# Optimization experiments

Measured on AMD Instinct MI355X. Metric: run time of the kernel, lower is better.

Reference implementation:

```python
import jax, jax.numpy as jnp
import numpy as np

N_HEAD = 16
D_MODEL = 1024
B, C = 4, 2048

def setup_inputs() -> dict:
    key = jax.random.key(0)
    k_x, k_wq, k_bq, k_wo, k_bo = jax.random.split(key, 5)
    s = 0.02
    return {
        "x": jax.random.normal(k_x, (B, C, D_MODEL), dtype=jnp.float32),
        "W_qkv": jax.random.normal(k_wq, (D_MODEL, 3 * D_MODEL), dtype=jnp.float32) * s,
        "b_qkv": jax.random.normal(k_bq, (3 * D_MODEL,), dtype=jnp.float32) * s,
        "W_o": jax.random.normal(k_wo, (D_MODEL, D_MODEL), dtype=jnp.float32) * s,
        "b_o": jax.random.normal(k_bo, (D_MODEL,), dtype=jnp.float32) * s,
    }

def reference(x, W_qkv, b_qkv, W_o, b_o):
    Bsz, Cq, D = x.shape
    H = N_HEAD
    hd = D // H
    qkv = x @ W_qkv + b_qkv                      # [B,C,3D]
    Q, K, V = jnp.split(qkv, 3, axis=2)
    # [B,C,H,hd] -> [B,H,C,hd]
    Q = Q.reshape(Bsz, Cq, H, hd).transpose(0, 2, 1, 3)
    K = K.reshape(Bsz, Cq, H, hd).transpose(0, 2, 1, 3)
    V = V.reshape(Bsz, Cq, H, hd).transpose(0, 2, 1, 3)
    scale = 1.0 / np.sqrt(hd).astype(np.float32)
    att = jnp.einsum('bhqd,bhkd->bhqk', Q, K) * scale
    causal = jnp.tril(jnp.ones((Cq, Cq), dtype=bool))
    att = jnp.where(causal, att, jnp.float32(-jnp.inf))
    att = jax.nn.softmax(att, axis=-1)           # dropout = identity (eval)
    out = jnp.einsum('bhqk,bhkd->bhqd', att, V)  # [B,H,C,hd]
    out = out.transpose(0, 2, 1, 3).reshape(Bsz, Cq, D)
    return out @ W_o + b_o
```

## Files before the change

### kernel.cpp

```cpp
#include <hip/hip_runtime.h>
#include <hip/hip_bf16.h>

typedef __attribute__((ext_vector_type(8))) short bf16x8;
typedef __attribute__((ext_vector_type(4))) float f32x4;

#define NH 16
#define DM 1024
#define HD 64
#define CSEQ 2048
#define MROWS 8192
#define NBH 64

static __device__ __forceinline__ unsigned short f2bf(float f) {
  __hip_bfloat16 h = __float2bfloat16(f);
  return *reinterpret_cast<unsigned short*>(&h);
}

static __device__ __forceinline__ short bf_qscale(short s) {
  unsigned u = ((unsigned)(unsigned short)s) << 16;
  float f = __builtin_bit_cast(float, u) * 0.18033688f;
  return (short)f2bf(f);
}

static __device__ __forceinline__ void gload_lds16(const void* g, void* l) {
  __builtin_amdgcn_global_load_lds(
      (const __attribute__((address_space(1))) unsigned int*)g,
      (__attribute__((address_space(3))) unsigned int*)l, 16, 0, 0);
}

__global__ __launch_bounds__(256) void cast_f32_bf16(const float* __restrict__ in,
                                                     unsigned short* __restrict__ out,
                                                     int n4) {
  int stride = gridDim.x * blockDim.x;
  for (int i = blockIdx.x * blockDim.x + threadIdx.x; i < n4; i += stride) {
    float4 v = ((const float4*)in)[i];
    ushort4 o;
    o.x = f2bf(v.x); o.y = f2bf(v.y); o.z = f2bf(v.z); o.w = f2bf(v.w);
    ((ushort4*)out)[i] = o;
  }
}

__global__ __launch_bounds__(256) void transpose_cast(const float* __restrict__ src,
                                                      unsigned short* __restrict__ dst,
                                                      int K, int N) {
  __shared__ float tile[32][33];
  int tx = threadIdx.x, ty = threadIdx.y;
  int n0 = blockIdx.x * 32, k0 = blockIdx.y * 32;
  #pragma unroll
  for (int i = 0; i < 32; i += 8)
    tile[ty + i][tx] = src[(size_t)(k0 + ty + i) * N + n0 + tx];
  __syncthreads();
  #pragma unroll
  for (int i = 0; i < 32; i += 8)
    dst[(size_t)(n0 + ty + i) * K + k0 + tx] = f2bf(tile[tx][ty + i]);
}


static __device__ __forceinline__ void stage_half(const unsigned short* s0,
                                                  const unsigned short* s1,
                                                  char* dst, int c0, int c1) {
  gload_lds16(s0, dst + c0 * 16);
  gload_lds16(s1, dst + c1 * 16);
}

template<int CNT>
static __device__ __forceinline__ void ld_frags(const char* base, int r0, int cx, int g,
                                                bf16x8 (*out)[2]) {
  #pragma unroll
  for (int i = 0; i < CNT; i++) {
    int row = r0 + i * 16 + cx;
    #pragma unroll
    for (int kc = 0; kc < 2; kc++)
      out[i][kc] = *(const bf16x8*)(base + row * 128 + ((((kc << 2) | g) ^ (row & 7)) << 4));
  }
}

static __device__ __forceinline__ void mfma_q(const bf16x8 af[4][2], const bf16x8 bfr[2][2],
                                              f32x4 acc[8][4], int qm, int qn) {
  #pragma unroll
  for (int kc = 0; kc < 2; kc++)
    #pragma unroll
    for (int mi = 0; mi < 4; mi++)
      #pragma unroll
      for (int ni = 0; ni < 2; ni++)
        acc[qm * 4 + mi][qn * 2 + ni] = __builtin_amdgcn_mfma_f32_16x16x32_bf16(
            af[mi][kc], bfr[ni][kc], acc[qm * 4 + mi][qn * 2 + ni], 0, 0, 0);
}

#define BARR() __builtin_amdgcn_s_barrier()
#define LGKM0() asm volatile("s_waitcnt lgkmcnt(0)" ::: "memory")
#define PRIO1() __builtin_amdgcn_s_setprio(1)
#define PRIO0() __builtin_amdgcn_s_setprio(0)

template<int MODE>
__global__ __launch_bounds__(512, 2) void gemm256(const unsigned short* __restrict__ A,
                                                  const unsigned short* __restrict__ BT,
                                                  const float* __restrict__ bias,
                                                  float* __restrict__ outF,
                                                  unsigned short* __restrict__ outQKV,
                                                  int N, int K) {
  __shared__ char sA[2][32768];
  __shared__ char sB[2][32768];
  int tid = threadIdx.x;
  int w = tid >> 6, l = tid & 63, g = l >> 4, cx = l & 15;
  int wm = (w >> 2) * 128, wn = (w & 3) * 64;

  int nwgx = gridDim.x;
  int nwg = nwgx * gridDim.y;
  int gid = blockIdx.y * nwgx + blockIdx.x;
  int swz = (gid & 7) * (nwg >> 3) + (gid >> 3);
  int bm = (swz / nwgx) * 256, bn = (swz % nwgx) * 256;

  int c0 = tid, c1 = tid + 512;
  int ar0 = c0 >> 3, as0 = ((c0 & 7) ^ (ar0 & 7)) * 8;
  int ar1 = c1 >> 3, as1 = ((c1 & 7) ^ (ar1 & 7)) * 8;
  const unsigned short* Ap0 = A + (size_t)(bm + ar0) * K + as0;
  const unsigned short* Ap1 = A + (size_t)(bm + ar1) * K + as1;
  const unsigned short* Bp0 = BT + (size_t)(bn + ar0) * K + as0;
  const unsigned short* Bp1 = BT + (size_t)(bn + ar1) * K + as1;
  const size_t HS = (size_t)128 * K;

  f32x4 acc[8][4];
  #pragma unroll
  for (int i = 0; i < 8; i++)
    #pragma unroll
    for (int j = 0; j < 4; j++) acc[i][j] = (f32x4){0.f, 0.f, 0.f, 0.f};

  int NT = K >> 6;

  stage_half(Ap0,      Ap1,      sA[0],         c0, c1);
  stage_half(Ap0 + HS, Ap1 + HS, sA[0] + 16384, c0, c1);
  stage_half(Bp0,      Bp1,      sB[0],         c0, c1);
  stage_half(Bp0 + HS, Bp1 + HS, sB[0] + 16384, c0, c1);
  stage_half(Ap0 + 64, Ap1 + 64, sA[1],         c0, c1);
  asm volatile("s_waitcnt vmcnt(2)" ::: "memory");
  BARR();

  int cur = 0;
  for (int t = 0; t < NT; t++) {
    const char* Ac = sA[cur];
    const char* Bc = sB[cur];
    char* An = sA[cur ^ 1];
    char* Bn = sB[cur ^ 1];
    int kn  = (t + 1) << 6;
    int kn2 = (t + 2) << 6;
    bool h1 = (t + 1) < NT, h2 = (t + 2) < NT;
    bf16x8 af[4][2], bfr[2][2];

    ld_frags<4>(Ac, wm, cx, g, af);
    ld_frags<2>(Bc, wn, cx, g, bfr);
    if (h1) stage_half(Ap0 + HS + kn, Ap1 + HS + kn, An + 16384, c0, c1);
    BARR(); LGKM0();
    PRIO1(); mfma_q(af, bfr, acc, 0, 0); PRIO0();
    BARR();

    ld_frags<2>(Bc, wn + 32, cx, g, bfr);
    if (h1) stage_half(Bp0 + kn, Bp1 + kn, Bn, c0, c1);
    BARR(); LGKM0();
    PRIO1(); mfma_q(af, bfr, acc, 0, 1); PRIO0();
    BARR();

    ld_frags<4>(Ac, wm + 64, cx, g, af);
    ld_frags<2>(Bc, wn, cx, g, bfr);
    if (h1) stage_half(Bp0 + HS + kn, Bp1 + HS + kn, Bn + 16384, c0, c1);
    BARR(); LGKM0();
    PRIO1(); mfma_q(af, bfr, acc, 1, 0); PRIO0();
    BARR();

    ld_frags<2>(Bc, wn + 32, cx, g, bfr);
    BARR(); LGKM0();
    if (h2) stage_half(Ap0 + kn2, Ap1 + kn2, sA[cur], c0, c1);
    PRIO1(); mfma_q(af, bfr, acc, 1, 1); PRIO0();
    if (h1) {
      if (h2) { asm volatile("s_waitcnt vmcnt(2)" ::: "memory"); }
      else    { asm volatile("s_waitcnt vmcnt(0)" ::: "memory"); }
    }
    BARR();
    cur ^= 1;
  }

  #pragma unroll
  for (int ai = 0; ai < 8; ai++) {
    #pragma unroll
    for (int aj = 0; aj < 4; aj++) {
      int col = bn + wn + aj * 16 + cx;
      float bv = bias[col];
      int row0 = bm + wm + ai * 16 + g * 4;
      #pragma unroll
      for (int r = 0; r < 4; r++) {
        float v = acc[ai][aj][r] + bv;
        int rr = row0 + r;
        if (MODE == 0) {
          outF[(size_t)rr * N + col] = v;
        } else {
          int which = col >> 10, rem = col & 1023;
          int h = rem >> 6, d = rem & 63;
          int b = rr >> 11, cq = rr & 2047;
          if (which == 2) {
            int pos = (cq & ~31) + (((cq >> 2) & 3) << 3) + (((cq >> 4) & 1) << 2) + (cq & 3);
            outQKV[((size_t)2 * NBH + b * NH + h) * (CSEQ * HD) +
                   (size_t)d * CSEQ + pos] = f2bf(v);
          } else {
            outQKV[((size_t)which * NBH + b * NH + h) * (CSEQ * HD) + (size_t)cq * HD + d] = f2bf(v);
          }
        }
      }
    }
  }
}

__global__ __launch_bounds__(512, 4) void attn_kernel(const unsigned short* __restrict__ Qb,
                                                      const unsigned short* __restrict__ Kb,
                                                      const unsigned short* __restrict__ VTb,
                                                      unsigned short* __restrict__ O) {
  __shared__ char sKb[2][16384];
  __shared__ char sVt[2][16384];
  int tid = threadIdx.x;
  int w = tid >> 6, l = tid & 63, g = l >> 4, cx = l & 15;
  int gid = blockIdx.x;
  int bh = ((gid >> 7) << 3) | (gid & 7);
  int qt = 15 - ((gid >> 3) & 15);

  const unsigned short* Qp  = Qb  + (size_t)bh * CSEQ * HD;
  const unsigned short* Kp  = Kb  + (size_t)bh * CSEQ * HD;
  const unsigned short* VTp = VTb + (size_t)bh * CSEQ * HD;

  int qrow = qt * 128 + w * 16 + cx;
  bf16x8 qf[2];
  qf[0] = *(const bf16x8*)(Qp + (size_t)qrow * HD + g * 8);
  qf[1] = *(const bf16x8*)(Qp + (size_t)qrow * HD + 32 + g * 8);
  #pragma unroll
  for (int kc = 0; kc < 2; kc++)
    #pragma unroll
    for (int j = 0; j < 8; j++) qf[kc][j] = bf_qscale(qf[kc][j]);

  f32x4 o[4];
  #pragma unroll
  for (int nf2 = 0; nf2 < 4; nf2++) o[nf2] = (f32x4){0.f, 0.f, 0.f, 0.f};
  float mrow = -INFINITY, lrow = 0.f;

  int c0 = tid, c1 = tid + 512;
  int krow0 = c0 >> 3, ksl0 = (c0 & 7) ^ (krow0 & 7);
  int krow1 = c1 >> 3, ksl1 = (c1 & 7) ^ (krow1 & 7);
  int vd0 = c0 >> 4, vsl0 = (c0 & 15) ^ (vd0 & 7);
  int vd1 = c1 >> 4, vsl1 = (c1 & 15) ^ (vd1 & 7);
  const unsigned short* Ksrc0 = Kp + (size_t)krow0 * HD + ksl0 * 8;
  const unsigned short* Ksrc1 = Kp + (size_t)krow1 * HD + ksl1 * 8;
  const unsigned short* Vsrc0 = VTp + (size_t)vd0 * CSEQ + vsl0 * 8;
  const unsigned short* Vsrc1 = VTp + (size_t)vd1 * CSEQ + vsl1 * 8;

  gload_lds16(Ksrc0, sKb[0] + c0 * 16);
  gload_lds16(Ksrc1, sKb[0] + c1 * 16);
  gload_lds16(Vsrc0, sVt[0] + c0 * 16);
  gload_lds16(Vsrc1, sVt[0] + c1 * 16);
  __syncthreads();
  int cur = 0;

  for (int kt = 0; kt <= qt; kt++) {
    if (kt < qt) {
      size_t ko = (size_t)(kt + 1) * 128 * HD;
      size_t vo = (size_t)(kt + 1) * 128;
      gload_lds16(Ksrc0 + ko, sKb[cur ^ 1] + c0 * 16);
      gload_lds16(Ksrc1 + ko, sKb[cur ^ 1] + c1 * 16);
      gload_lds16(Vsrc0 + vo, sVt[cur ^ 1] + c0 * 16);
      gload_lds16(Vsrc1 + vo, sVt[cur ^ 1] + c1 * 16);
    }
    const char* Kc = sKb[cur];
    const char* Vc = sVt[cur];

    f32x4 sacc[8];
    #pragma unroll
    for (int nf = 0; nf < 8; nf++) sacc[nf] = (f32x4){0.f, 0.f, 0.f, 0.f};
    __builtin_amdgcn_s_setprio(1);
    #pragma unroll
    for (int kc = 0; kc < 2; kc++) {
      #pragma unroll
      for (int nf = 0; nf < 8; nf++) {
        int row = nf * 16 + cx;
        bf16x8 kf = *(const bf16x8*)(Kc + row * 128 + ((((kc << 2) | g) ^ (row & 7)) << 4));
        sacc[nf] = __builtin_amdgcn_mfma_f32_16x16x32_bf16(kf, qf[kc], sacc[nf], 0, 0, 0);
      }
    }
    __builtin_amdgcn_s_setprio(0);

    if (kt == qt) {
      #pragma unroll
      for (int nf = 0; nf < 8; nf++)
        #pragma unroll
        for (int r = 0; r < 4; r++)
          if (nf * 16 + 4 * g + r > w * 16 + cx) sacc[nf][r] = -INFINITY;
    }
    float m8[8];
    #pragma unroll
    for (int nf = 0; nf < 8; nf++)
      m8[nf] = fmaxf(fmaxf(sacc[nf][0], sacc[nf][1]), fmaxf(sacc[nf][2], sacc[nf][3]));
    float mx = fmaxf(fmaxf(fmaxf(m8[0], m8[1]), fmaxf(m8[2], m8[3])),
                     fmaxf(fmaxf(m8[4], m8[5]), fmaxf(m8[6], m8[7])));
    mx = fmaxf(mx, __shfl_xor(mx, 16));
    mx = fmaxf(mx, __shfl_xor(mx, 32));

    if (!__all(mx - mrow <= 8.f)) {
      float mnew = fmaxf(mrow, mx);
      float alpha = __builtin_amdgcn_exp2f(mrow - mnew);
      mrow = mnew;
      lrow *= alpha;
      #pragma unroll
      for (int r = 0; r < 4; r++) {
        float ar = __shfl(alpha, (l & 48) | ((l >> 2) & 12) | r);
        #pragma unroll
        for (int nf2 = 0; nf2 < 4; nf2++) o[nf2][r] *= ar;
      }
    }
    #pragma unroll
    for (int nf = 0; nf < 8; nf++)
      #pragma unroll
      for (int r = 0; r < 4; r++)
        sacc[nf][r] = __builtin_amdgcn_exp2f(sacc[nf][r] - mrow);
    float s8[8];
    #pragma unroll
    for (int nf = 0; nf < 8; nf++)
      s8[nf] = (sacc[nf][0] + sacc[nf][1]) + (sacc[nf][2] + sacc[nf][3]);
    float sum = ((s8[0] + s8[1]) + (s8[2] + s8[3])) + ((s8[4] + s8[5]) + (s8[6] + s8[7]));
    sum += __shfl_xor(sum, 16);
    sum += __shfl_xor(sum, 32);
    lrow += sum;

    bf16x8 pa[4];
    #pragma unroll
    for (int kc = 0; kc < 4; kc++) {
      #pragma unroll
      for (int j = 0; j < 4; j++) {
        pa[kc][j]     = (short)f2bf(sacc[2 * kc][j]);
        pa[kc][j + 4] = (short)f2bf(sacc[2 * kc + 1][j]);
      }
    }

    __builtin_amdgcn_s_setprio(1);
    #pragma unroll
    for (int kc = 0; kc < 4; kc++) {
      #pragma unroll
      for (int nf2 = 0; nf2 < 4; nf2++) {
        int d = nf2 * 16 + cx;
        bf16x8 vf = *(const bf16x8*)(Vc + ((d * 256 + (((kc << 2) | g) << 4)) ^ ((d & 7) << 4)));
        o[nf2] = __builtin_amdgcn_mfma_f32_16x16x32_bf16(pa[kc], vf, o[nf2], 0, 0, 0);
      }
    }
    __builtin_amdgcn_s_setprio(0);

    if (kt < qt) {
      __syncthreads();
      cur ^= 1;
    }
  }

  int b = bh >> 4, h = bh & 15;
  float linv = 1.0f / lrow;
  #pragma unroll
  for (int r = 0; r < 4; r++) {
    float inv = __shfl(linv, (l & 48) | ((l >> 2) & 12) | r);
    int q = qt * 128 + w * 16 + 4 * g + r;
    size_t base = ((size_t)(b * CSEQ + q)) * DM + h * HD;
    #pragma unroll
    for (int nf2 = 0; nf2 < 4; nf2++)
      O[base + nf2 * 16 + cx] = f2bf(o[nf2][r] * inv);
  }
}

extern "C" void kernel_launch(void* const* d_in, const int* in_sizes, int n_in,
                              void* d_out, int out_size, void* d_ws, size_t ws_size,
                              hipStream_t stream) {
  const float* x    = (const float*)d_in[0];
  const float* Wqkv = (const float*)d_in[1];
  const float* bqkv = (const float*)d_in[2];
  const float* Wo   = (const float*)d_in[3];
  const float* bo   = (const float*)d_in[4];
  float* out = (float*)d_out;

  unsigned short* ws = (unsigned short*)d_ws;
  const size_t XB_OFF    = 0;
  const size_t WQKVT_OFF = 8388608;
  const size_t WOT_OFF   = WQKVT_OFF + 3145728;
  const size_t QKV_OFF   = WOT_OFF + 1048576;
  const size_t ATT_OFF   = QKV_OFF + 3 * 8388608;

  unsigned short* xb    = ws + XB_OFF;
  unsigned short* wqkvT = ws + WQKVT_OFF;
  unsigned short* woT   = ws + WOT_OFF;
  unsigned short* qkv   = ws + QKV_OFF;
  unsigned short* att   = ws + ATT_OFF;

  cast_f32_bf16<<<2048, 256, 0, stream>>>(x, xb, (MROWS * DM) / 4);
  transpose_cast<<<dim3(3 * DM / 32, DM / 32), dim3(32, 8), 0, stream>>>(Wqkv, wqkvT, DM, 3 * DM);
  transpose_cast<<<dim3(DM / 32, DM / 32), dim3(32, 8), 0, stream>>>(Wo, woT, DM, DM);

  gemm256<1><<<dim3(3 * DM / 256, MROWS / 256), 512, 0, stream>>>(
      xb, wqkvT, bqkv, nullptr, qkv, 3 * DM, DM);

  attn_kernel<<<dim3(1024), 512, 0, stream>>>(
      qkv, qkv + 8388608, qkv + 16777216, att);

  gemm256<0><<<dim3(DM / 256, MROWS / 256), 512, 0, stream>>>(
      att, woT, bo, out, nullptr, DM, DM);
}
```

Measured before the change: 225.0 us.

## Shrink GEMM tile to 256x128 with 4x2 wave layout and two-phase pipeline

The GEMM block tile changes from 256x256 to 256x128. The 8 waves are rearranged into a 4x2 grid, each owning a 64x64 sub-tile, so per-wave accumulators drop from 128 to 64 floats and B shared memory is halved. The k-loop is reorganized into two MFMA phases with new staging and vmcnt accounting, and the launch grids are doubled. This doubles the block count (notably for the output projection, 128 to 256 blocks), improving occupancy and wave balance across CUs, at the cost of lower arithmetic intensity per block and more A-tile reloads.

```diff
diff --git a/kernel.cpp b/kernel.cpp
--- a/kernel.cpp
+++ b/kernel.cpp
@@ -56,13 +56,6 @@
 }
 
 
-static __device__ __forceinline__ void stage_half(const unsigned short* s0,
-                                                  const unsigned short* s1,
-                                                  char* dst, int c0, int c1) {
-  gload_lds16(s0, dst + c0 * 16);
-  gload_lds16(s1, dst + c1 * 16);
-}
-
 template<int CNT>
 static __device__ __forceinline__ void ld_frags(const char* base, int r0, int cx, int g,
                                                 bf16x8 (*out)[2]) {
@@ -75,20 +68,22 @@
   }
 }
 
-static __device__ __forceinline__ void mfma_q(const bf16x8 af[4][2], const bf16x8 bfr[2][2],
-                                              f32x4 acc[8][4], int qm, int qn) {
+static __device__ __forceinline__ void mfma_pair(const bf16x8 af[4][2], const bf16x8 bf2[2][2],
+                                                 f32x4 acc[4][4], int n0) {
   #pragma unroll
   for (int kc = 0; kc < 2; kc++)
     #pragma unroll
     for (int mi = 0; mi < 4; mi++)
       #pragma unroll
       for (int ni = 0; ni < 2; ni++)
-        acc[qm * 4 + mi][qn * 2 + ni] = __builtin_amdgcn_mfma_f32_16x16x32_bf16(
-            af[mi][kc], bfr[ni][kc], acc[qm * 4 + mi][qn * 2 + ni], 0, 0, 0);
+        acc[mi][n0 + ni] = __builtin_amdgcn_mfma_f32_16x16x32_bf16(
+            af[mi][kc], bf2[ni][kc], acc[mi][n0 + ni], 0, 0, 0);
 }
 
 #define BARR() __builtin_amdgcn_s_barrier()
 #define LGKM0() asm volatile("s_waitcnt lgkmcnt(0)" ::: "memory")
+#define VMCNT4() asm volatile("s_waitcnt vmcnt(4)" ::: "memory")
+#define VMCNT0() asm volatile("s_waitcnt vmcnt(0)" ::: "memory")
 #define PRIO1() __builtin_amdgcn_s_setprio(1)
 #define PRIO0() __builtin_amdgcn_s_setprio(0)
 
@@ -100,16 +95,16 @@
                                                   unsigned short* __restrict__ outQKV,
                                                   int N, int K) {
   __shared__ char sA[2][32768];
-  __shared__ char sB[2][32768];
+  __shared__ char sB[2][16384];
   int tid = threadIdx.x;
   int w = tid >> 6, l = tid & 63, g = l >> 4, cx = l & 15;
-  int wm = (w >> 2) * 128, wn = (w & 3) * 64;
+  int wm = (w >> 1) * 64, wn = (w & 1) * 64;
 
   int nwgx = gridDim.x;
   int nwg = nwgx * gridDim.y;
   int gid = blockIdx.y * nwgx + blockIdx.x;
   int swz = (gid & 7) * (nwg >> 3) + (gid >> 3);
-  int bm = (swz / nwgx) * 256, bn = (swz % nwgx) * 256;
+  int bm = (swz / nwgx) * 256, bn = (swz % nwgx) * 128;
 
   int c0 = tid, c1 = tid + 512;
   int ar0 = c0 >> 3, as0 = ((c0 & 7) ^ (ar0 & 7)) * 8;
@@ -120,75 +115,63 @@
   const unsigned short* Bp1 = BT + (size_t)(bn + ar1) * K + as1;
   const size_t HS = (size_t)128 * K;
 
-  f32x4 acc[8][4];
-  #pragma unroll
-  for (int i = 0; i < 8; i++)
+  #define STAGE_A(t, buf) do { int ko = (t) << 6;                       \
+      gload_lds16(Ap0 + ko,      sA[buf] + c0 * 16);                    \
+      gload_lds16(Ap1 + ko,      sA[buf] + c1 * 16);                    \
+      gload_lds16(Ap0 + HS + ko, sA[buf] + 16384 + c0 * 16);            \
+      gload_lds16(Ap1 + HS + ko, sA[buf] + 16384 + c1 * 16); } while (0)
+  #define STAGE_B(t, buf) do { int ko = (t) << 6;                       \
+      gload_lds16(Bp0 + ko, sB[buf] + c0 * 16);                         \
+      gload_lds16(Bp1 + ko, sB[buf] + c1 * 16); } while (0)
+
+  f32x4 acc[4][4];
+  #pragma unroll
+  for (int i = 0; i < 4; i++)
     #pragma unroll
     for (int j = 0; j < 4; j++) acc[i][j] = (f32x4){0.f, 0.f, 0.f, 0.f};
 
   int NT = K >> 6;
 
-  stage_half(Ap0,      Ap1,      sA[0],         c0, c1);
-  stage_half(Ap0 + HS, Ap1 + HS, sA[0] + 16384, c0, c1);
-  stage_half(Bp0,      Bp1,      sB[0],         c0, c1);
-  stage_half(Bp0 + HS, Bp1 + HS, sB[0] + 16384, c0, c1);
-  stage_half(Ap0 + 64, Ap1 + 64, sA[1],         c0, c1);
-  asm volatile("s_waitcnt vmcnt(2)" ::: "memory");
+  STAGE_A(0, 0);
+  STAGE_B(0, 0);
+  STAGE_A(1, 1);
+  VMCNT4();
   BARR();
 
   int cur = 0;
   for (int t = 0; t < NT; t++) {
     const char* Ac = sA[cur];
     const char* Bc = sB[cur];
-    char* An = sA[cur ^ 1];
-    char* Bn = sB[cur ^ 1];
-    int kn  = (t + 1) << 6;
-    int kn2 = (t + 2) << 6;
     bool h1 = (t + 1) < NT, h2 = (t + 2) < NT;
-    bf16x8 af[4][2], bfr[2][2];
+    bf16x8 af[4][2], bfr[4][2];
 
     ld_frags<4>(Ac, wm, cx, g, af);
-    ld_frags<2>(Bc, wn, cx, g, bfr);
-    if (h1) stage_half(Ap0 + HS + kn, Ap1 + HS + kn, An + 16384, c0, c1);
+    ld_frags<2>(Bc, wn, cx, g, &bfr[0]);
+    if (h1) STAGE_B(t + 1, cur ^ 1);
     BARR(); LGKM0();
-    PRIO1(); mfma_q(af, bfr, acc, 0, 0); PRIO0();
+    PRIO1(); mfma_pair(af, &bfr[0], acc, 0); PRIO0();
     BARR();
 
-    ld_frags<2>(Bc, wn + 32, cx, g, bfr);
-    if (h1) stage_half(Bp0 + kn, Bp1 + kn, Bn, c0, c1);
+    ld_frags<2>(Bc, wn + 32, cx, g, &bfr[2]);
+    if (h2) STAGE_A(t + 2, cur);
     BARR(); LGKM0();
-    PRIO1(); mfma_q(af, bfr, acc, 0, 1); PRIO0();
-    BARR();
-
-    ld_frags<4>(Ac, wm + 64, cx, g, af);
-    ld_frags<2>(Bc, wn, cx, g, bfr);
-    if (h1) stage_half(Bp0 + HS + kn, Bp1 + HS + kn, Bn + 16384, c0, c1);
-    BARR(); LGKM0();
-    PRIO1(); mfma_q(af, bfr, acc, 1, 0); PRIO0();
-    BARR();
-
-    ld_frags<2>(Bc, wn + 32, cx, g, bfr);
-    BARR(); LGKM0();
-    if (h2) stage_half(Ap0 + kn2, Ap1 + kn2, sA[cur], c0, c1);
-    PRIO1(); mfma_q(af, bfr, acc, 1, 1); PRIO0();
-    if (h1) {
-      if (h2) { asm volatile("s_waitcnt vmcnt(2)" ::: "memory"); }
-      else    { asm volatile("s_waitcnt vmcnt(0)" ::: "memory"); }
-    }
+    PRIO1(); mfma_pair(af, &bfr[2], acc, 2); PRIO0();
+    if (h2)      { VMCNT4(); }
+    else if (h1) { VMCNT0(); }
     BARR();
     cur ^= 1;
   }
 
   #pragma unroll
-  for (int ai = 0; ai < 8; ai++) {
-    #pragma unroll
-    for (int aj = 0; aj < 4; aj++) {
-      int col = bn + wn + aj * 16 + cx;
+  for (int mi = 0; mi < 4; mi++) {
+    #pragma unroll
+    for (int ni = 0; ni < 4; ni++) {
+      int col = bn + wn + ni * 16 + cx;
       float bv = bias[col];
-      int row0 = bm + wm + ai * 16 + g * 4;
+      int row0 = bm + wm + mi * 16 + g * 4;
       #pragma unroll
       for (int r = 0; r < 4; r++) {
-        float v = acc[ai][aj][r] + bv;
+        float v = acc[mi][ni][r] + bv;
         int rr = row0 + r;
         if (MODE == 0) {
           outF[(size_t)rr * N + col] = v;
@@ -207,6 +190,8 @@
       }
     }
   }
+  #undef STAGE_A
+  #undef STAGE_B
 }
 
 __global__ __launch_bounds__(512, 4) void attn_kernel(const unsigned short* __restrict__ Qb,
@@ -393,12 +378,12 @@
   transpose_cast<<<dim3(3 * DM / 32, DM / 32), dim3(32, 8), 0, stream>>>(Wqkv, wqkvT, DM, 3 * DM);
   transpose_cast<<<dim3(DM / 32, DM / 32), dim3(32, 8), 0, stream>>>(Wo, woT, DM, DM);
 
-  gemm256<1><<<dim3(3 * DM / 256, MROWS / 256), 512, 0, stream>>>(
+  gemm256<1><<<dim3(3 * DM / 128, MROWS / 256), 512, 0, stream>>>(
       xb, wqkvT, bqkv, nullptr, qkv, 3 * DM, DM);
 
   attn_kernel<<<dim3(1024), 512, 0, stream>>>(
       qkv, qkv + 8388608, qkv + 16777216, att);
 
-  gemm256<0><<<dim3(DM / 256, MROWS / 256), 512, 0, stream>>>(
+  gemm256<0><<<dim3(DM / 128, MROWS / 256), 512, 0, stream>>>(
       att, woT, bo, out, nullptr, DM, DM);
 }
```

Measured after the change: 201.4 us. 10.5% less time.
